# Kernel optimization log

Measured on AMD Instinct MI355X. Metric: run time of the kernel, lower is better.

Reference implementation:

```python
import jax, jax.numpy as jnp
import numpy as np

N_NODES = 200000
N_EDGES = 1600000
N_GRAPHS = 2000
IN_DIM, W1_DIM, W2_DIM, N_CLASSES = 8, 64, 12, 2


def setup_inputs() -> dict:
    key = jax.random.key(0)
    ks = jax.random.split(key, 9)
    x = jax.random.normal(ks[0], (N_NODES, IN_DIM), dtype=jnp.float32)
    edge_index = jax.random.randint(ks[1], (2, N_EDGES), 0, N_NODES, dtype=jnp.int64)
    batch_index = jnp.sort(jax.random.randint(ks[2], (N_NODES,), 0, N_GRAPHS, dtype=jnp.int64))
    # Glorot-ish scaled params
    W1 = jax.random.normal(ks[3], (IN_DIM, W1_DIM), dtype=jnp.float32) * (1.0 / np.sqrt(IN_DIM))
    b1 = jnp.zeros((W1_DIM,), dtype=jnp.float32)
    W2 = jax.random.normal(ks[4], (W1_DIM, W2_DIM), dtype=jnp.float32) * (1.0 / np.sqrt(W1_DIM))
    b2 = jnp.zeros((W2_DIM,), dtype=jnp.float32)
    Wl = jax.random.normal(ks[5], (W2_DIM, N_CLASSES), dtype=jnp.float32) * (1.0 / np.sqrt(W2_DIM))
    bl = jnp.zeros((N_CLASSES,), dtype=jnp.float32)
    return {"x": x, "edge_index": edge_index, "batch_index": batch_index,
            "W1": W1, "b1": b1, "W2": W2, "b2": b2, "Wl": Wl, "bl": bl}


def _gcn_conv(x, W, b, src, dst, deg_inv_sqrt, n_nodes):
    # x' = D^{-1/2} (A + I) D^{-1/2} X W + b  (self-loops already in src/dst)
    xw = x @ W                                   # [N, out]
    norm = deg_inv_sqrt[src] * deg_inv_sqrt[dst]  # [E+N]
    msg = xw[src] * norm[:, None]                 # edge-wise gather (memory-bound)
    out = jax.ops.segment_sum(msg, dst, num_segments=n_nodes)
    return out + b


def reference(x, edge_index, batch_index, W1, b1, W2, b2, Wl, bl):
    n = x.shape[0]
    loops = jnp.arange(n, dtype=edge_index.dtype)
    src = jnp.concatenate([edge_index[0], loops])
    dst = jnp.concatenate([edge_index[1], loops])
    # degree (with self-loops) on destination nodes, as in PyG gcn_norm
    deg = jax.ops.segment_sum(jnp.ones_like(dst, dtype=x.dtype), dst, num_segments=n)
    deg_inv_sqrt = jax.lax.rsqrt(deg)  # deg >= 1 due to self-loops
    h = jax.nn.relu(_gcn_conv(x, W1, b1, src, dst, deg_inv_sqrt, n))
    h = jax.nn.relu(_gcn_conv(h, W2, b2, src, dst, deg_inv_sqrt, n))
    pooled = jax.ops.segment_max(h, batch_index, num_segments=N_GRAPHS)  # global_max_pool
    logits = pooled @ Wl + bl
    return jax.nn.log_softmax(logits, axis=1)
```

## Files before the change

kernel.cpp:

```cpp
#include <hip/hip_runtime.h>
#include <hip/hip_fp16.h>
#include <stdint.h>


constexpr int IN_DIM = 8;
constexpr int H1 = 64;
constexpr int H2 = 12;
constexpr int NPB = 512;
constexpr int NBK = 391;
constexpr int CAP = 4608;
constexpr int CHUNK = 4096;
constexpr int SLOTS = 16;

typedef float nfloat4 __attribute__((ext_vector_type(4)));
__device__ __forceinline__ void nt_store_f4(void* p, float4 v) {
    nfloat4 w = {v.x, v.y, v.z, v.w};
    __builtin_nontemporal_store(w, (nfloat4*)p);
}

__device__ __forceinline__ float4 h2x2_to_f4(int2 rv) {
    __half2 a = *(__half2*)&rv.x;
    __half2 b = *(__half2*)&rv.y;
    float2 fa = __half22float2(a), fb = __half22float2(b);
    return make_float4(fa.x, fa.y, fb.x, fb.y);
}

__global__ void k_binA(const int* __restrict__ src, const int* __restrict__ dst,
                       uint32_t* __restrict__ pairs, int* __restrict__ bcursor, int ne) {
    __shared__ int s_cur[NBK];
    __shared__ int s_gb[NBK];
    for (int i = threadIdx.x; i < NBK; i += 256) s_cur[i] = 0;
    __syncthreads();
    int e0 = blockIdx.x * CHUNK;
    int rec[16];
#pragma unroll
    for (int i = 0; i < 16; ++i) {
        int e = e0 + i * 256 + threadIdx.x;
        rec[i] = -1;
        if (e < ne) {
            int d = __builtin_nontemporal_load(&dst[e]);
            int b = d >> 9;
            int off = atomicAdd(&s_cur[b], 1);
            rec[i] = (off << 18) | ((d & 511) << 9) | b;
        }
    }
    __syncthreads();
    for (int b = threadIdx.x; b < NBK; b += 256) {
        int c = s_cur[b];
        s_gb[b] = (c > 0) ? atomicAdd(&bcursor[b], c) : 0;
    }
    __syncthreads();
#pragma unroll
    for (int i = 0; i < 16; ++i) {
        if (rec[i] < 0) continue;
        int e = e0 + i * 256 + threadIdx.x;
        int b = rec[i] & 511;
        int dl = (rec[i] >> 9) & 511;
        int off = (rec[i] >> 18) + s_gb[b];
        if (off < CAP)
            pairs[(size_t)b * CAP + off] =
                ((uint32_t)dl << 18) | (uint32_t)__builtin_nontemporal_load(&src[e]);
    }
}

__global__ void __launch_bounds__(256) k_binB(
        const uint32_t* __restrict__ pairs, const int* __restrict__ bcursor,
        const float* __restrict__ x, int* __restrict__ csr_pad,
        int* __restrict__ csr_ovf, unsigned int* __restrict__ meta,
        float* __restrict__ dis, __half2* __restrict__ xdh, int n) {
    __shared__ int s_hist[NPB];
    __shared__ int s_start[NPB];
    __shared__ int s_cur[NPB];
    __shared__ int s_tmp[256];
    __shared__ int s_pad[NPB * SLOTS];
    int b = blockIdx.x;
    int t = threadIdx.x;
    int cnt = min(bcursor[b], CAP);
    const uint32_t* pb = pairs + (size_t)b * CAP;
    for (int i = t; i < NPB; i += 256) { s_hist[i] = 0; s_cur[i] = 0; }
    for (int i = t; i < NPB * SLOTS; i += 256) s_pad[i] = n;
    __syncthreads();
    for (int i = t; i < cnt; i += 256)
        atomicAdd(&s_hist[__builtin_nontemporal_load(&pb[i]) >> 18], 1);
    __syncthreads();
    int b2i = t * 2;
    int v0 = s_hist[b2i], v1 = s_hist[b2i + 1];
    int tot = v0 + v1;
    s_tmp[t] = tot;
    __syncthreads();
    for (int off = 1; off < 256; off <<= 1) {
        int u = (t >= off) ? s_tmp[t - off] : 0;
        __syncthreads();
        s_tmp[t] += u;
        __syncthreads();
    }
    int ex = s_tmp[t] - tot;
    s_start[b2i] = ex;
    s_start[b2i + 1] = ex + v0;
    __syncthreads();
    int cb = b * CAP;
    int node0 = b << 9;
    for (int i = t; i < NPB; i += 256) {
        int node = node0 + i;
        if (node < n) {
            meta[node] = ((unsigned int)s_hist[i] << 21) | (unsigned int)(cb + s_start[i]);
            float di = rsqrtf((float)(s_hist[i] + 1));
            dis[node] = di;
            const float4* xi = (const float4*)(x + (size_t)node * IN_DIM);
            float4 a = xi[0], c = xi[1];
            union { __half2 h[4]; int iv[4]; } u;
            u.h[0] = __float22half2_rn(make_float2(a.x * di, a.y * di));
            u.h[1] = __float22half2_rn(make_float2(a.z * di, a.w * di));
            u.h[2] = __float22half2_rn(make_float2(c.x * di, c.y * di));
            u.h[3] = __float22half2_rn(make_float2(c.z * di, c.w * di));
            ((int4*)xdh)[node] = make_int4(u.iv[0], u.iv[1], u.iv[2], u.iv[3]);
        } else if (node == n) {
            ((int4*)xdh)[n] = make_int4(0, 0, 0, 0);
        }
    }
    __syncthreads();
    for (int i = t; i < cnt; i += 256) {
        uint32_t p = __builtin_nontemporal_load(&pb[i]);
        int dl = p >> 18;
        int sidx = (int)(p & 0x3FFFFu);
        int pos = atomicAdd(&s_cur[dl], 1);
        if (pos < SLOTS) s_pad[dl * SLOTS + pos] = sidx;
        else             csr_ovf[cb + s_start[dl] + pos] = sidx;
    }
    __syncthreads();
    for (int i = t; i < NPB * SLOTS / 4; i += 256) {
        int node = node0 + (i >> 2);
        if (node < n)
            ((int4*)csr_pad)[(size_t)node0 * 4 + i] = ((int4*)s_pad)[i];
    }
}

__global__ void k_agg1(const int* __restrict__ csr_pad, const int* __restrict__ csr_ovf,
                       const unsigned int* __restrict__ meta, const __half2* __restrict__ xdh,
                       const float* __restrict__ dis, float* __restrict__ z1, int n) {
    int wid = blockIdx.x * 4 + (threadIdx.x >> 6);
    int node0 = wid * 4;
    if (node0 >= n) return;
    int lane = threadIdx.x & 63;
    int ns = lane >> 4;
    int sl = lane & 15;
    int node = node0 + ns;
    int d2 = sl & 1;
    int rsub = sl >> 1;
    int padv = __builtin_nontemporal_load(&csr_pad[(size_t)node0 * SLOTS + lane]);
    unsigned int m = meta[node];
    float4 acc = make_float4(0.f, 0.f, 0.f, 0.f);
#pragma unroll
    for (int i = 0; i < 3; ++i) {
        int r = 8 * i + rsub;
        int nb = __shfl(padv, (ns << 4) | (r & 15), 64);
        nb = (r < SLOTS) ? nb : ((r == SLOTS) ? node : n);
        int2 rv = ((const int2*)(xdh + (size_t)nb * 4))[d2];
        float4 f = h2x2_to_f4(rv);
        acc.x += f.x; acc.y += f.y; acc.z += f.z; acc.w += f.w;
    }
    int deg = m >> 21;
    if (deg > SLOTS) {
        int r0 = m & 0x1FFFFF;
        for (int r = SLOTS + rsub; r < deg; r += 8) {
            int nb = csr_ovf[r0 + r];
            int2 rv = ((const int2*)(xdh + (size_t)nb * 4))[d2];
            float4 f = h2x2_to_f4(rv);
            acc.x += f.x; acc.y += f.y; acc.z += f.z; acc.w += f.w;
        }
    }
#pragma unroll
    for (int mk = 2; mk <= 8; mk <<= 1) {
        acc.x += __shfl_xor(acc.x, mk, 64);
        acc.y += __shfl_xor(acc.y, mk, 64);
        acc.z += __shfl_xor(acc.z, mk, 64);
        acc.w += __shfl_xor(acc.w, mk, 64);
    }
    if (rsub == 0) {
        float di = dis[node];
        nt_store_f4(z1 + (size_t)node * 8 + d2 * 4,
                    make_float4(acc.x * di, acc.y * di, acc.z * di, acc.w * di));
    }
}

__device__ __forceinline__ void fma4(float4& a, float s, const float4 w) {
    a.x = fmaf(s, w.x, a.x); a.y = fmaf(s, w.y, a.y);
    a.z = fmaf(s, w.z, a.z); a.w = fmaf(s, w.w, a.w);
}

__global__ void k_fused(const float* __restrict__ z1, const float* __restrict__ dis,
                        const float* __restrict__ W1, const float* __restrict__ b1,
                        const float* __restrict__ W2, __half2* __restrict__ y2h, int n) {
    __shared__ float sW1[IN_DIM * H1];
    __shared__ float sW2[H1 * H2];
    __shared__ float sb1[H1];
    for (int i = threadIdx.x; i < IN_DIM * H1; i += 256) sW1[i] = W1[i];
    for (int i = threadIdx.x; i < H1 * H2; i += 256) sW2[i] = W2[i];
    if (threadIdx.x < H1) sb1[threadIdx.x] = b1[threadIdx.x];
    __syncthreads();
    int node = blockIdx.x * 256 + threadIdx.x;
    if (node > n) return;
    int4* orow = (int4*)y2h + (size_t)node * 2;
    if (node == n) {
        orow[0] = make_int4(0, 0, 0, 0);
        orow[1] = make_int4(0, 0, 0, 0);
        return;
    }
    const float4* z4 = (const float4*)(z1 + (size_t)node * IN_DIM);
    float4 za = z4[0], zb = z4[1];
    float z[8] = {za.x, za.y, za.z, za.w, zb.x, zb.y, zb.z, zb.w};

    const float4* w1v = (const float4*)sW1;
    const float4* b1v = (const float4*)sb1;
    float4 h[16];
#pragma unroll
    for (int d4 = 0; d4 < 16; ++d4) h[d4] = b1v[d4];
#pragma unroll
    for (int k = 0; k < IN_DIM; ++k) {
        float zk = z[k];
#pragma unroll
        for (int d4 = 0; d4 < 16; ++d4) fma4(h[d4], zk, w1v[k * 16 + d4]);
    }
#pragma unroll
    for (int d4 = 0; d4 < 16; ++d4) {
        h[d4].x = fmaxf(h[d4].x, 0.f); h[d4].y = fmaxf(h[d4].y, 0.f);
        h[d4].z = fmaxf(h[d4].z, 0.f); h[d4].w = fmaxf(h[d4].w, 0.f);
    }
    const float4* w2v = (const float4*)sW2;
    float4 acc0 = {0, 0, 0, 0}, acc1 = {0, 0, 0, 0}, acc2 = {0, 0, 0, 0};
#pragma unroll
    for (int d4 = 0; d4 < 16; ++d4) {
        float el[4] = {h[d4].x, h[d4].y, h[d4].z, h[d4].w};
#pragma unroll
        for (int c = 0; c < 4; ++c) {
            int d = d4 * 4 + c;
            fma4(acc0, el[c], w2v[d * 3 + 0]);
            fma4(acc1, el[c], w2v[d * 3 + 1]);
            fma4(acc2, el[c], w2v[d * 3 + 2]);
        }
    }
    float di = dis[node];
    union { __half2 h2v[8]; int iv[8]; } u;
    u.h2v[0] = __float22half2_rn(make_float2(acc0.x * di, acc0.y * di));
    u.h2v[1] = __float22half2_rn(make_float2(acc0.z * di, acc0.w * di));
    u.h2v[2] = __float22half2_rn(make_float2(acc1.x * di, acc1.y * di));
    u.h2v[3] = __float22half2_rn(make_float2(acc1.z * di, acc1.w * di));
    u.h2v[4] = __float22half2_rn(make_float2(acc2.x * di, acc2.y * di));
    u.h2v[5] = __float22half2_rn(make_float2(acc2.z * di, acc2.w * di));
    u.h2v[6] = __float22half2_rn(make_float2(0.f, 0.f));
    u.h2v[7] = __float22half2_rn(make_float2(0.f, 0.f));
    orow[0] = make_int4(u.iv[0], u.iv[1], u.iv[2], u.iv[3]);
    orow[1] = make_int4(u.iv[4], u.iv[5], u.iv[6], u.iv[7]);
}

__global__ void k_agg2(const int* __restrict__ csr_pad, const int* __restrict__ csr_ovf,
                       const unsigned int* __restrict__ meta, const __half2* __restrict__ y2h,
                       const float* __restrict__ dis, const float* __restrict__ b2,
                       float* __restrict__ h2, int n) {
    int wid = blockIdx.x * 4 + (threadIdx.x >> 6);
    int node0 = wid * 4;
    if (node0 >= n) return;
    int lane = threadIdx.x & 63;
    int ns = lane >> 4;
    int sl = lane & 15;
    int node = node0 + ns;
    int c = sl & 3;
    int rsub = sl >> 2;
    int padv = __builtin_nontemporal_load(&csr_pad[(size_t)node0 * SLOTS + lane]);
    unsigned int m = meta[node];
    float4 acc = make_float4(0.f, 0.f, 0.f, 0.f);
#pragma unroll
    for (int i = 0; i < 5; ++i) {
        int r = 4 * i + rsub;
        int nb = __shfl(padv, (ns << 4) | (r & 15), 64);
        nb = (r < SLOTS) ? nb : ((r == SLOTS) ? node : n);
        int2 rv = ((const int2*)(y2h + (size_t)nb * 8))[c];
        float4 f = h2x2_to_f4(rv);
        acc.x += f.x; acc.y += f.y; acc.z += f.z; acc.w += f.w;
    }
    int deg = m >> 21;
    if (deg > SLOTS) {
        int r0 = m & 0x1FFFFF;
        for (int r = SLOTS + rsub; r < deg; r += 4) {
            int nb = csr_ovf[r0 + r];
            int2 rv = ((const int2*)(y2h + (size_t)nb * 8))[c];
            float4 f = h2x2_to_f4(rv);
            acc.x += f.x; acc.y += f.y; acc.z += f.z; acc.w += f.w;
        }
    }
#pragma unroll
    for (int mk = 4; mk <= 8; mk <<= 1) {
        acc.x += __shfl_xor(acc.x, mk, 64);
        acc.y += __shfl_xor(acc.y, mk, 64);
        acc.z += __shfl_xor(acc.z, mk, 64);
        acc.w += __shfl_xor(acc.w, mk, 64);
    }
    if (rsub == 0 && c < 3) {
        float di = dis[node];
        float4 bb = ((const float4*)b2)[c];
        float4 v;
        v.x = fmaxf(fmaf(acc.x, di, bb.x), 0.f);
        v.y = fmaxf(fmaf(acc.y, di, bb.y), 0.f);
        v.z = fmaxf(fmaf(acc.z, di, bb.z), 0.f);
        v.w = fmaxf(fmaf(acc.w, di, bb.w), 0.f);
        nt_store_f4(h2 + (size_t)node * H2 + c * 4, v);
    }
}

__global__ void __launch_bounds__(128) k_pool(
        const float* __restrict__ h2, const int* __restrict__ batch,
        const float* __restrict__ Wl, const float* __restrict__ bl,
        float* __restrict__ out, int n) {
    __shared__ float s_m[120];
    __shared__ float s_p[12];
    __shared__ int s_be[2];
    int g = blockIdx.x;
    int t = threadIdx.x;
    if (t < 2) {
        int target = g + t;
        int lo = 0, hi = n;
        while (lo < hi) {
            int mid = (lo + hi) >> 1;
            if (batch[mid] < target) lo = mid + 1; else hi = mid;
        }
        s_be[t] = lo;
    }
    __syncthreads();
    int gs = s_be[0], ge = s_be[1];
    if (t < 120) {
        int off = t / 12, dim = t - off * 12;
        float m = 0.f;
        for (int i = gs + off; i < ge; i += 10)
            m = fmaxf(m, h2[(size_t)i * 12 + dim]);
        s_m[t] = m;
    }
    __syncthreads();
    if (t < 12) {
        float m = s_m[t];
#pragma unroll
        for (int k = 1; k < 10; ++k) m = fmaxf(m, s_m[t + 12 * k]);
        s_p[t] = m;
    }
    __syncthreads();
    if (t == 0) {
        float l0 = bl[0], l1 = bl[1];
#pragma unroll
        for (int k = 0; k < H2; ++k) {
            float pv = s_p[k];
            l0 = fmaf(pv, Wl[k * 2 + 0], l0);
            l1 = fmaf(pv, Wl[k * 2 + 1], l1);
        }
        float m = fmaxf(l0, l1);
        float lse = m + logf(expf(l0 - m) + expf(l1 - m));
        out[g * 2 + 0] = l0 - lse;
        out[g * 2 + 1] = l1 - lse;
    }
}

extern "C" void kernel_launch(void* const* d_in, const int* in_sizes, int n_in,
                              void* d_out, int out_size, void* d_ws, size_t ws_size,
                              hipStream_t stream) {
    const float* x   = (const float*)d_in[0];
    const int* ei    = (const int*)d_in[1];
    const int* batch = (const int*)d_in[2];
    const float* W1  = (const float*)d_in[3];
    const float* b1  = (const float*)d_in[4];
    const float* W2  = (const float*)d_in[5];
    const float* b2  = (const float*)d_in[6];
    const float* Wl  = (const float*)d_in[7];
    const float* bl  = (const float*)d_in[8];
    float* out = (float*)d_out;

    const int N = in_sizes[0] / IN_DIM;
    const int E = in_sizes[1] / 2;
    const int G = out_size / 2;
    const int* src = ei;
    const int* dst = ei + E;

    auto cdiv = [](long long a, int b) { return (int)((a + b - 1) / b); };

    char* wp = (char*)d_ws;
    auto carve = [&](size_t bytes) {
        char* p = wp;
        wp += (bytes + 63) & ~(size_t)63;
        return p;
    };
    int*          bcursor = (int*)carve(NBK * 4);
    unsigned int* meta    = (unsigned int*)carve((size_t)N * 4);
    float*        dis     = (float*)carve((size_t)N * 4);
    __half2*      xdh     = (__half2*)carve((size_t)(N + 1) * 16);
    float*        z1      = (float*)carve((size_t)N * IN_DIM * 4);
    __half2*      y2h     = (__half2*)carve((size_t)(N + 1) * 32);
    float*        h2      = (float*)carve((size_t)N * H2 * 4);
    uint32_t*     pairs   = (uint32_t*)carve((size_t)NBK * CAP * 4);
    int*          csr_pad = (int*)carve((size_t)N * SLOTS * 4);
    int*          csr_ovf = (int*)carve((size_t)NBK * CAP * 4);

    (void)hipMemsetAsync(bcursor, 0, NBK * sizeof(int), stream);

    k_binA<<<cdiv(E, CHUNK), 256, 0, stream>>>(src, dst, pairs, bcursor, E);
    k_binB<<<NBK, 256, 0, stream>>>(pairs, bcursor, x, csr_pad, csr_ovf,
                                    meta, dis, xdh, N);

    k_agg1<<<cdiv(N, 16), 256, 0, stream>>>(csr_pad, csr_ovf, meta, xdh, dis, z1, N);
    k_fused<<<cdiv((long long)N + 1, 256), 256, 0, stream>>>(z1, dis, W1, b1, W2, y2h, N);
    k_agg2<<<cdiv(N, 16), 256, 0, stream>>>(csr_pad, csr_ovf, meta, y2h, dis, b2, h2, N);
    k_pool<<<G, 128, 0, stream>>>(h2, batch, Wl, bl, out, N);
}
```

Before: 192.0 us.

## Fuse layer-1 aggregation into the MLP kernel and use thread-per-node gathers

Merges the first-layer neighbor aggregation into the dense W1/ReLU/W2 kernel, so the z1 intermediate buffer and one launch go away. Both aggregation kernels switch from 16 lanes per node with shuffle reductions to one thread per node that reads the padded CSR row as int4 and gathers whole half-precision feature rows. This drops the shuffle overhead and the z1 round trip through memory. In exchange, per-thread gathers become less coalesced, and high-degree nodes run a serial overflow loop.

```diff
diff --git a/kernel.cpp b/kernel.cpp
--- a/kernel.cpp
+++ b/kernel.cpp
@@ -18,11 +18,13 @@
     __builtin_nontemporal_store(w, (nfloat4*)p);
 }
 
-__device__ __forceinline__ float4 h2x2_to_f4(int2 rv) {
-    __half2 a = *(__half2*)&rv.x;
-    __half2 b = *(__half2*)&rv.y;
-    float2 fa = __half22float2(a), fb = __half22float2(b);
-    return make_float4(fa.x, fa.y, fb.x, fb.y);
+__device__ __forceinline__ void acc_row8(float* acc, int4 rv) {
+    const __half2* h = (const __half2*)&rv;
+#pragma unroll
+    for (int q = 0; q < 4; ++q) {
+        float2 f = __half22float2(h[q]);
+        acc[2 * q] += f.x; acc[2 * q + 1] += f.y;
+    }
 }
 
 __global__ void k_binA(const int* __restrict__ src, const int* __restrict__ dst,
@@ -135,62 +137,12 @@
     }
 }
 
-__global__ void k_agg1(const int* __restrict__ csr_pad, const int* __restrict__ csr_ovf,
-                       const unsigned int* __restrict__ meta, const __half2* __restrict__ xdh,
-                       const float* __restrict__ dis, float* __restrict__ z1, int n) {
-    int wid = blockIdx.x * 4 + (threadIdx.x >> 6);
-    int node0 = wid * 4;
-    if (node0 >= n) return;
-    int lane = threadIdx.x & 63;
-    int ns = lane >> 4;
-    int sl = lane & 15;
-    int node = node0 + ns;
-    int d2 = sl & 1;
-    int rsub = sl >> 1;
-    int padv = __builtin_nontemporal_load(&csr_pad[(size_t)node0 * SLOTS + lane]);
-    unsigned int m = meta[node];
-    float4 acc = make_float4(0.f, 0.f, 0.f, 0.f);
-#pragma unroll
-    for (int i = 0; i < 3; ++i) {
-        int r = 8 * i + rsub;
-        int nb = __shfl(padv, (ns << 4) | (r & 15), 64);
-        nb = (r < SLOTS) ? nb : ((r == SLOTS) ? node : n);
-        int2 rv = ((const int2*)(xdh + (size_t)nb * 4))[d2];
-        float4 f = h2x2_to_f4(rv);
-        acc.x += f.x; acc.y += f.y; acc.z += f.z; acc.w += f.w;
-    }
-    int deg = m >> 21;
-    if (deg > SLOTS) {
-        int r0 = m & 0x1FFFFF;
-        for (int r = SLOTS + rsub; r < deg; r += 8) {
-            int nb = csr_ovf[r0 + r];
-            int2 rv = ((const int2*)(xdh + (size_t)nb * 4))[d2];
-            float4 f = h2x2_to_f4(rv);
-            acc.x += f.x; acc.y += f.y; acc.z += f.z; acc.w += f.w;
-        }
-    }
-#pragma unroll
-    for (int mk = 2; mk <= 8; mk <<= 1) {
-        acc.x += __shfl_xor(acc.x, mk, 64);
-        acc.y += __shfl_xor(acc.y, mk, 64);
-        acc.z += __shfl_xor(acc.z, mk, 64);
-        acc.w += __shfl_xor(acc.w, mk, 64);
-    }
-    if (rsub == 0) {
-        float di = dis[node];
-        nt_store_f4(z1 + (size_t)node * 8 + d2 * 4,
-                    make_float4(acc.x * di, acc.y * di, acc.z * di, acc.w * di));
-    }
-}
-
-__device__ __forceinline__ void fma4(float4& a, float s, const float4 w) {
-    a.x = fmaf(s, w.x, a.x); a.y = fmaf(s, w.y, a.y);
-    a.z = fmaf(s, w.z, a.z); a.w = fmaf(s, w.w, a.w);
-}
-
-__global__ void k_fused(const float* __restrict__ z1, const float* __restrict__ dis,
-                        const float* __restrict__ W1, const float* __restrict__ b1,
-                        const float* __restrict__ W2, __half2* __restrict__ y2h, int n) {
+__global__ void __launch_bounds__(256) k_agg1f(
+        const int* __restrict__ csr_pad, const int* __restrict__ csr_ovf,
+        const unsigned int* __restrict__ meta, const __half2* __restrict__ xdh,
+        const float* __restrict__ dis, const float* __restrict__ W1,
+        const float* __restrict__ b1, const float* __restrict__ W2,
+        __half2* __restrict__ y2h, int n) {
     __shared__ float sW1[IN_DIM * H1];
     __shared__ float sW2[H1 * H2];
     __shared__ float sb1[H1];
@@ -206,105 +158,105 @@
         orow[1] = make_int4(0, 0, 0, 0);
         return;
     }
-    const float4* z4 = (const float4*)(z1 + (size_t)node * IN_DIM);
-    float4 za = z4[0], zb = z4[1];
-    float z[8] = {za.x, za.y, za.z, za.w, zb.x, zb.y, zb.z, zb.w};
-
-    const float4* w1v = (const float4*)sW1;
-    const float4* b1v = (const float4*)sb1;
-    float4 h[16];
-#pragma unroll
-    for (int d4 = 0; d4 < 16; ++d4) h[d4] = b1v[d4];
-#pragma unroll
-    for (int k = 0; k < IN_DIM; ++k) {
-        float zk = z[k];
-#pragma unroll
-        for (int d4 = 0; d4 < 16; ++d4) fma4(h[d4], zk, w1v[k * 16 + d4]);
-    }
-#pragma unroll
-    for (int d4 = 0; d4 < 16; ++d4) {
-        h[d4].x = fmaxf(h[d4].x, 0.f); h[d4].y = fmaxf(h[d4].y, 0.f);
-        h[d4].z = fmaxf(h[d4].z, 0.f); h[d4].w = fmaxf(h[d4].w, 0.f);
-    }
-    const float4* w2v = (const float4*)sW2;
-    float4 acc0 = {0, 0, 0, 0}, acc1 = {0, 0, 0, 0}, acc2 = {0, 0, 0, 0};
-#pragma unroll
-    for (int d4 = 0; d4 < 16; ++d4) {
-        float el[4] = {h[d4].x, h[d4].y, h[d4].z, h[d4].w};
-#pragma unroll
-        for (int c = 0; c < 4; ++c) {
-            int d = d4 * 4 + c;
-            fma4(acc0, el[c], w2v[d * 3 + 0]);
-            fma4(acc1, el[c], w2v[d * 3 + 1]);
-            fma4(acc2, el[c], w2v[d * 3 + 2]);
-        }
+    const int4* pr = (const int4*)(csr_pad + (size_t)node * SLOTS);
+    int4 p0 = pr[0], p1 = pr[1], p2 = pr[2], p3 = pr[3];
+    unsigned int m = meta[node];
+    const int4* xt = (const int4*)xdh;
+
+    float acc[8] = {0, 0, 0, 0, 0, 0, 0, 0};
+    int idx[16] = {p0.x, p0.y, p0.z, p0.w, p1.x, p1.y, p1.z, p1.w,
+                   p2.x, p2.y, p2.z, p2.w, p3.x, p3.y, p3.z, p3.w};
+    acc_row8(acc, xt[node]);
+#pragma unroll
+    for (int i = 0; i < 16; ++i) acc_row8(acc, xt[(size_t)idx[i]]);
+    int deg = m >> 21;
+    if (deg > SLOTS) {
+        int r0 = (int)(m & 0x1FFFFF);
+        for (int r = SLOTS; r < deg; ++r) acc_row8(acc, xt[(size_t)csr_ovf[r0 + r]]);
     }
     float di = dis[node];
+    float z[8];
+#pragma unroll
+    for (int k = 0; k < 8; ++k) z[k] = acc[k] * di;
+
+    float y2[H2];
+#pragma unroll
+    for (int j = 0; j < H2; ++j) y2[j] = 0.f;
+    for (int d = 0; d < H1; ++d) {
+        float h = sb1[d];
+#pragma unroll
+        for (int k = 0; k < 8; ++k) h = fmaf(z[k], sW1[k * H1 + d], h);
+        h = fmaxf(h, 0.f);
+#pragma unroll
+        for (int j = 0; j < H2; ++j) y2[j] = fmaf(h, sW2[d * H2 + j], y2[j]);
+    }
     union { __half2 h2v[8]; int iv[8]; } u;
-    u.h2v[0] = __float22half2_rn(make_float2(acc0.x * di, acc0.y * di));
-    u.h2v[1] = __float22half2_rn(make_float2(acc0.z * di, acc0.w * di));
-    u.h2v[2] = __float22half2_rn(make_float2(acc1.x * di, acc1.y * di));
-    u.h2v[3] = __float22half2_rn(make_float2(acc1.z * di, acc1.w * di));
-    u.h2v[4] = __float22half2_rn(make_float2(acc2.x * di, acc2.y * di));
-    u.h2v[5] = __float22half2_rn(make_float2(acc2.z * di, acc2.w * di));
+#pragma unroll
+    for (int q = 0; q < 6; ++q)
+        u.h2v[q] = __float22half2_rn(make_float2(y2[2 * q] * di, y2[2 * q + 1] * di));
     u.h2v[6] = __float22half2_rn(make_float2(0.f, 0.f));
-    u.h2v[7] = __float22half2_rn(make_float2(0.f, 0.f));
+    u.h2v[7] = u.h2v[6];
     orow[0] = make_int4(u.iv[0], u.iv[1], u.iv[2], u.iv[3]);
     orow[1] = make_int4(u.iv[4], u.iv[5], u.iv[6], u.iv[7]);
 }
 
-__global__ void k_agg2(const int* __restrict__ csr_pad, const int* __restrict__ csr_ovf,
-                       const unsigned int* __restrict__ meta, const __half2* __restrict__ y2h,
-                       const float* __restrict__ dis, const float* __restrict__ b2,
-                       float* __restrict__ h2, int n) {
-    int wid = blockIdx.x * 4 + (threadIdx.x >> 6);
-    int node0 = wid * 4;
-    if (node0 >= n) return;
-    int lane = threadIdx.x & 63;
-    int ns = lane >> 4;
-    int sl = lane & 15;
-    int node = node0 + ns;
-    int c = sl & 3;
-    int rsub = sl >> 2;
-    int padv = __builtin_nontemporal_load(&csr_pad[(size_t)node0 * SLOTS + lane]);
+__global__ void __launch_bounds__(256) k_agg2(
+        const int* __restrict__ csr_pad, const int* __restrict__ csr_ovf,
+        const unsigned int* __restrict__ meta, const __half2* __restrict__ y2h,
+        const float* __restrict__ dis, const float* __restrict__ b2,
+        float* __restrict__ h2, int n) {
+    int node = blockIdx.x * 256 + threadIdx.x;
+    if (node >= n) return;
+    const int4* pr = (const int4*)(csr_pad + (size_t)node * SLOTS);
+    int4 p0 = pr[0], p1 = pr[1], p2 = pr[2], p3 = pr[3];
     unsigned int m = meta[node];
-    float4 acc = make_float4(0.f, 0.f, 0.f, 0.f);
-#pragma unroll
-    for (int i = 0; i < 5; ++i) {
-        int r = 4 * i + rsub;
-        int nb = __shfl(padv, (ns << 4) | (r & 15), 64);
-        nb = (r < SLOTS) ? nb : ((r == SLOTS) ? node : n);
-        int2 rv = ((const int2*)(y2h + (size_t)nb * 8))[c];
-        float4 f = h2x2_to_f4(rv);
-        acc.x += f.x; acc.y += f.y; acc.z += f.z; acc.w += f.w;
-    }
+    const int4* yt = (const int4*)y2h;
+
+    float acc[12] = {0, 0, 0, 0, 0, 0, 0, 0, 0, 0, 0, 0};
+    auto addrow = [&](int nb) {
+        int4 ra = yt[(size_t)nb * 2];
+        int4 rb = yt[(size_t)nb * 2 + 1];
+        const __half2* ha = (const __half2*)&ra;
+        const __half2* hb = (const __half2*)&rb;
+#pragma unroll
+        for (int q = 0; q < 4; ++q) {
+            float2 f = __half22float2(ha[q]);
+            acc[2 * q] += f.x; acc[2 * q + 1] += f.y;
+        }
+#pragma unroll
+        for (int q = 0; q < 2; ++q) {
+            float2 f = __half22float2(hb[q]);
+            acc[8 + 2 * q] += f.x; acc[9 + 2 * q] += f.y;
+        }
+    };
+    int idx[16] = {p0.x, p0.y, p0.z, p0.w, p1.x, p1.y, p1.z, p1.w,
+                   p2.x, p2.y, p2.z, p2.w, p3.x, p3.y, p3.z, p3.w};
+    addrow(node);
+#pragma unroll
+    for (int i = 0; i < 16; ++i) addrow(idx[i]);
     int deg = m >> 21;
     if (deg > SLOTS) {
-        int r0 = m & 0x1FFFFF;
-        for (int r = SLOTS + rsub; r < deg; r += 4) {
-            int nb = csr_ovf[r0 + r];
-            int2 rv = ((const int2*)(y2h + (size_t)nb * 8))[c];
-            float4 f = h2x2_to_f4(rv);
-            acc.x += f.x; acc.y += f.y; acc.z += f.z; acc.w += f.w;
-        }
-    }
-#pragma unroll
-    for (int mk = 4; mk <= 8; mk <<= 1) {
-        acc.x += __shfl_xor(acc.x, mk, 64);
-        acc.y += __shfl_xor(acc.y, mk, 64);
-        acc.z += __shfl_xor(acc.z, mk, 64);
-        acc.w += __shfl_xor(acc.w, mk, 64);
-    }
-    if (rsub == 0 && c < 3) {
-        float di = dis[node];
-        float4 bb = ((const float4*)b2)[c];
-        float4 v;
-        v.x = fmaxf(fmaf(acc.x, di, bb.x), 0.f);
-        v.y = fmaxf(fmaf(acc.y, di, bb.y), 0.f);
-        v.z = fmaxf(fmaf(acc.z, di, bb.z), 0.f);
-        v.w = fmaxf(fmaf(acc.w, di, bb.w), 0.f);
-        nt_store_f4(h2 + (size_t)node * H2 + c * 4, v);
-    }
+        int r0 = (int)(m & 0x1FFFFF);
+        for (int r = SLOTS; r < deg; ++r) addrow(csr_ovf[r0 + r]);
+    }
+    float di = dis[node];
+    float4 v0, v1, v2;
+    v0.x = fmaxf(fmaf(acc[0], di, b2[0]), 0.f);
+    v0.y = fmaxf(fmaf(acc[1], di, b2[1]), 0.f);
+    v0.z = fmaxf(fmaf(acc[2], di, b2[2]), 0.f);
+    v0.w = fmaxf(fmaf(acc[3], di, b2[3]), 0.f);
+    v1.x = fmaxf(fmaf(acc[4], di, b2[4]), 0.f);
+    v1.y = fmaxf(fmaf(acc[5], di, b2[5]), 0.f);
+    v1.z = fmaxf(fmaf(acc[6], di, b2[6]), 0.f);
+    v1.w = fmaxf(fmaf(acc[7], di, b2[7]), 0.f);
+    v2.x = fmaxf(fmaf(acc[8], di, b2[8]), 0.f);
+    v2.y = fmaxf(fmaf(acc[9], di, b2[9]), 0.f);
+    v2.z = fmaxf(fmaf(acc[10], di, b2[10]), 0.f);
+    v2.w = fmaxf(fmaf(acc[11], di, b2[11]), 0.f);
+    float* o = h2 + (size_t)node * H2;
+    nt_store_f4(o, v0);
+    nt_store_f4(o + 4, v1);
+    nt_store_f4(o + 8, v2);
 }
 
 __global__ void __launch_bounds__(128) k_pool(
@@ -389,7 +341,6 @@
     unsigned int* meta    = (unsigned int*)carve((size_t)N * 4);
     float*        dis     = (float*)carve((size_t)N * 4);
     __half2*      xdh     = (__half2*)carve((size_t)(N + 1) * 16);
-    float*        z1      = (float*)carve((size_t)N * IN_DIM * 4);
     __half2*      y2h     = (__half2*)carve((size_t)(N + 1) * 32);
     float*        h2      = (float*)carve((size_t)N * H2 * 4);
     uint32_t*     pairs   = (uint32_t*)carve((size_t)NBK * CAP * 4);
@@ -402,8 +353,8 @@
     k_binB<<<NBK, 256, 0, stream>>>(pairs, bcursor, x, csr_pad, csr_ovf,
                                     meta, dis, xdh, N);
 
-    k_agg1<<<cdiv(N, 16), 256, 0, stream>>>(csr_pad, csr_ovf, meta, xdh, dis, z1, N);
-    k_fused<<<cdiv((long long)N + 1, 256), 256, 0, stream>>>(z1, dis, W1, b1, W2, y2h, N);
-    k_agg2<<<cdiv(N, 16), 256, 0, stream>>>(csr_pad, csr_ovf, meta, y2h, dis, b2, h2, N);
+    k_agg1f<<<cdiv((long long)N + 1, 256), 256, 0, stream>>>(
+        csr_pad, csr_ovf, meta, xdh, dis, W1, b1, W2, y2h, N);
+    k_agg2<<<cdiv(N, 256), 256, 0, stream>>>(csr_pad, csr_ovf, meta, y2h, dis, b2, h2, N);
     k_pool<<<G, 128, 0, stream>>>(h2, batch, Wl, bl, out, N);
 }
```

After: 192.7 us. Within noise of the previous version (+0.4%).
